# Performance work log

Measured on AMD Instinct MI355X. Metric: run time of the kernel, lower is better.

Reference implementation:

```python
import jax, jax.numpy as jnp
import numpy as np

N_NODES = 100_000
N_EDGES = 3_200_000
FAN_IN, FAN_MID, FAN_OUT = 512, 256, 64
NEG_SLOPE = 0.01  # F.leaky_relu default


def setup_inputs() -> dict:
    key = jax.random.key(0)
    ks = jax.random.split(key, 8)
    x = jax.random.normal(ks[0], (N_NODES, FAN_IN), dtype=jnp.float32)
    edge_src = jax.random.randint(ks[1], (N_EDGES,), 0, N_NODES, dtype=jnp.int32)
    edge_dst = jax.random.randint(ks[2], (N_EDGES,), 0, N_NODES, dtype=jnp.int32)
    edge_w1 = jax.random.uniform(ks[3], (N_EDGES,), dtype=jnp.float32)
    edge_w2 = jax.random.uniform(ks[4], (N_EDGES,), dtype=jnp.float32)
    W1 = jax.random.normal(ks[5], (FAN_IN, FAN_MID), dtype=jnp.float32) * (1.0 / np.sqrt(FAN_IN))
    b1 = jnp.zeros((FAN_MID,), dtype=jnp.float32)
    W2 = jax.random.normal(ks[6], (FAN_MID, FAN_OUT), dtype=jnp.float32) * (1.0 / np.sqrt(FAN_MID))
    b2 = jnp.zeros((FAN_OUT,), dtype=jnp.float32)
    return {"x": x, "edge_src": edge_src, "edge_dst": edge_dst,
            "edge_w1": edge_w1, "edge_w2": edge_w2,
            "W1": W1, "b1": b1, "W2": W2, "b2": b2}


def _gcn_layer(x, W, b, src, dst, ew):
    # GraphConvolution: support = x @ W ; out = A @ support + b (A sparse via edges)
    support = x @ W                                 # [N, F_out]
    msgs = support[src] * ew[:, None]               # gather + scale, [E, F_out]
    agg = jax.ops.segment_sum(msgs, dst, num_segments=x.shape[0])  # scatter-add
    return agg + b


def reference(x, edge_src, edge_dst, edge_w1, edge_w2, W1, b1, W2, b2):
    h = _gcn_layer(x, W1, b1, edge_src, edge_dst, edge_w1)
    h = jax.nn.leaky_relu(h, NEG_SLOPE)
    # dropout is identity at inference (training=False)
    h = _gcn_layer(h, W2, b2, edge_src, edge_dst, edge_w2)
    return jax.nn.log_softmax(h, axis=1)
```

## Files before the change

kernel.cpp:

```cpp
#include <hip/hip_runtime.h>
#include <stdint.h>

#define FAN_IN  512
#define FAN_MID 256
#define FAN_OUT 64
#define NEG_SLOPE 0.01f
#define NPB 128
#define MAXNB 1024
#define BPART 256

typedef __bf16 bf16_t;
typedef bf16_t bf16x8 __attribute__((ext_vector_type(8)));
typedef float  f32x4  __attribute__((ext_vector_type(4)));
typedef unsigned short u16x8 __attribute__((ext_vector_type(8)));

__device__ inline unsigned short f2b(float f) {
    union { float f; unsigned int u; } v; v.f = f;
    unsigned int u = v.u;
    return (unsigned short)((u + 0x7fffu + ((u >> 16) & 1u)) >> 16);
}
__device__ inline float b2f(unsigned short u) {
    union { unsigned int u; float f; } v; v.u = ((unsigned int)u) << 16; return v.f;
}

__global__ void zerob_kernel(int* p, int n) {
    int i = blockIdx.x * 256 + threadIdx.x;
    if (i < n) p[i] = 0;
}

__global__ __launch_bounds__(256) void part_hist(const int* __restrict__ dst,
                                                 int* __restrict__ gcount,
                                                 int* __restrict__ bcount,
                                                 int E, int nb, int chunk) {
    __shared__ int lc[MAXNB];
    int blk = blockIdx.x;
    for (int i = threadIdx.x; i < nb; i += 256) lc[i] = 0;
    __syncthreads();
    int s = blk * chunk;
    int e = s + chunk; if (e > E) e = E;
    for (int i = s + threadIdx.x; i < e; i += 256)
        atomicAdd(&lc[dst[i] >> 7], 1);
    __syncthreads();
    for (int i = threadIdx.x; i < nb; i += 256) {
        int c = lc[i];
        gcount[blk * nb + i] = c;
        if (c) atomicAdd(&bcount[i], c);
    }
}

__global__ void bscan_kernel(const int* __restrict__ bcount, int* __restrict__ boff,
                             int nb, int E) {
    __shared__ int part[1024];
    int t = threadIdx.x;
    int chunk = (nb + 1023) >> 10;
    int s = t * chunk;
    int e = s + chunk; if (e > nb) e = nb;
    int sum = 0;
    for (int i = s; i < e; i++) sum += bcount[i];
    part[t] = sum;
    __syncthreads();
    for (int off = 1; off < 1024; off <<= 1) {
        int v = (t >= off) ? part[t - off] : 0;
        __syncthreads();
        part[t] += v;
        __syncthreads();
    }
    int run = (t == 0) ? 0 : part[t - 1];
    for (int i = s; i < e; i++) {
        boff[i] = run;
        run += bcount[i];
    }
    if (t == 1023) boff[nb] = E;
}

__global__ __launch_bounds__(BPART) void part_scan(const int* __restrict__ gcount,
                                                   const int* __restrict__ boff,
                                                   int* __restrict__ gbase, int nb) {
    __shared__ int v[BPART];
    int bucket = blockIdx.x;
    int t = threadIdx.x;
    int val = gcount[t * nb + bucket];
    v[t] = val;
    __syncthreads();
    for (int off = 1; off < BPART; off <<= 1) {
        int x = (t >= off) ? v[t - off] : 0;
        __syncthreads();
        v[t] += x;
        __syncthreads();
    }
    gbase[t * nb + bucket] = (t == 0 ? 0 : v[t - 1]) + boff[bucket];
}

__global__ __launch_bounds__(256) void part_scatter(const int* __restrict__ src,
                                                    const int* __restrict__ dst,
                                                    const float* __restrict__ w1,
                                                    const float* __restrict__ w2,
                                                    const int* __restrict__ gbase,
                                                    uint4* __restrict__ bstage,
                                                    int E, int nb, int chunk) {
    __shared__ int lcur[MAXNB];
    int blk = blockIdx.x;
    for (int i = threadIdx.x; i < nb; i += 256) lcur[i] = gbase[blk * nb + i];
    __syncthreads();
    int s = blk * chunk;
    int e = s + chunk; if (e > E) e = E;
    for (int i = s + threadIdx.x; i < e; i += 256) {
        int d = dst[i];
        int pos = atomicAdd(&lcur[d >> 7], 1);
        uint4 v;
        v.x = (unsigned int)src[i];
        v.y = __float_as_uint(w1[i]);
        v.z = __float_as_uint(w2[i]);
        v.w = (unsigned int)d;
        bstage[pos] = v;
    }
}

__global__ __launch_bounds__(256) void bsort_kernel(const uint4* __restrict__ bstage,
                                                    const int* __restrict__ boff,
                                                    int* __restrict__ offsets,
                                                    uint4* __restrict__ csr,
                                                    int Nn, int E, int nb) {
    __shared__ int cnt[NPB];
    __shared__ int scn[NPB];
    __shared__ int cur[NPB];
    int b = blockIdx.x;
    int t = threadIdx.x;
    int base = boff[b], end = boff[b + 1];
    int n0 = b * NPB;
    if (t < NPB) cnt[t] = 0;
    __syncthreads();
    for (int i = base + t; i < end; i += 256)
        atomicAdd(&cnt[bstage[i].w - n0], 1);
    __syncthreads();
    if (t == 0) {
        int run = 0;
        for (int j = 0; j < NPB; j++) { scn[j] = run; run += cnt[j]; }
    }
    __syncthreads();
    if (t < NPB) {
        cur[t] = scn[t];
        int n = n0 + t;
        if (n < Nn) offsets[n] = base + scn[t];
    }
    if (b == nb - 1 && t == 0) offsets[Nn] = E;
    __syncthreads();
    for (int i = base + t; i < end; i += 256) {
        uint4 rec = bstage[i];
        int lp = atomicAdd(&cur[rec.w - n0], 1);
        csr[base + lp] = rec;
    }
}

__global__ void convert_w_kernel(const float* __restrict__ W, unsigned short* __restrict__ Wt,
                                 int K, int N) {
    int idx = blockIdx.x * 256 + threadIdx.x;
    if (idx >= K * N) return;
    int k = idx / N, n = idx % N;
    Wt[(size_t)n * K + k] = f2b(W[idx]);
}

template<int K, int N, bool A_F32>
__global__ __launch_bounds__(256) void gemm_bt(const void* __restrict__ Ap,
                                               const unsigned short* __restrict__ Bt,
                                               unsigned short* __restrict__ C, int M) {
    constexpr int LDT = 40;
    constexpr int NW  = N / 64;
    __shared__ unsigned short As[64 * LDT];
    __shared__ unsigned short Bs[N * LDT];
    const int m0   = blockIdx.x * 64;
    const int tid  = threadIdx.x;
    const int lane = tid & 63;
    const int w    = tid >> 6;
    const int lrow = tid >> 2;
    const int lseg = (tid & 3) * 8;
    const int q    = lane >> 4;
    const int mm   = lane & 15;

    f32x4 acc[4][NW] = {};

    for (int k0 = 0; k0 < K; k0 += 32) {
        __syncthreads();
        {
            int gm = m0 + lrow;
            u16x8 av;
            if (A_F32) {
                const float* A32 = (const float*)Ap;
                if (gm < M) {
                    const float4* pp = (const float4*)(A32 + (size_t)gm * K + k0 + lseg);
                    float4 f0 = pp[0], f1 = pp[1];
                    av[0] = f2b(f0.x); av[1] = f2b(f0.y); av[2] = f2b(f0.z); av[3] = f2b(f0.w);
                    av[4] = f2b(f1.x); av[5] = f2b(f1.y); av[6] = f2b(f1.z); av[7] = f2b(f1.w);
                } else av = (u16x8)0;
            } else {
                const unsigned short* A16 = (const unsigned short*)Ap;
                if (gm < M) av = *(const u16x8*)(A16 + (size_t)gm * K + k0 + lseg);
                else        av = (u16x8)0;
            }
            *(u16x8*)&As[lrow * LDT + lseg] = av;
        }
#pragma unroll
        for (int r = 0; r < N / 64; r++) {
            int nr = r * 64 + lrow;
            *(u16x8*)&Bs[nr * LDT + lseg] =
                *(const u16x8*)(Bt + (size_t)nr * K + k0 + lseg);
        }
        __syncthreads();

        bf16x8 a[4], b[NW];
#pragma unroll
        for (int mi = 0; mi < 4; mi++)
            a[mi] = *(const bf16x8*)&As[(mi * 16 + mm) * LDT + q * 8];
#pragma unroll
        for (int ni = 0; ni < NW; ni++)
            b[ni] = *(const bf16x8*)&Bs[(w * NW * 16 + ni * 16 + mm) * LDT + q * 8];
#pragma unroll
        for (int mi = 0; mi < 4; mi++)
#pragma unroll
            for (int ni = 0; ni < NW; ni++)
                acc[mi][ni] = __builtin_amdgcn_mfma_f32_16x16x32_bf16(a[mi], b[ni], acc[mi][ni], 0, 0, 0);
    }

#pragma unroll
    for (int mi = 0; mi < 4; mi++)
#pragma unroll
        for (int ni = 0; ni < NW; ni++)
#pragma unroll
            for (int r = 0; r < 4; r++) {
                int row = m0 + mi * 16 + q * 4 + r;
                if (row < M)
                    C[(size_t)row * N + w * NW * 16 + ni * 16 + mm] = f2b(acc[mi][ni][r]);
            }
}

__global__ __launch_bounds__(256) void agg1_kernel(const unsigned short* __restrict__ S,
                                                   const int* __restrict__ offsets,
                                                   const uint4* __restrict__ edges,
                                                   const float* __restrict__ b1,
                                                   unsigned short* __restrict__ h, int Nn) {
    int wave = threadIdx.x >> 6;
    int lane = threadIdx.x & 63;
    int node = blockIdx.x * 4 + wave;
    if (node >= Nn) return;
    int s = offsets[node], e = offsets[node + 1];
    float a0 = 0.f, a1 = 0.f, a2 = 0.f, a3 = 0.f;
    int i = s;
    for (; i + 4 <= e; i += 4) {
        uint4 e0 = edges[i], e1 = edges[i + 1], e2 = edges[i + 2], e3 = edges[i + 3];
        ushort4 v0 = *(const ushort4*)(S + (size_t)e0.x * 256 + lane * 4);
        ushort4 v1 = *(const ushort4*)(S + (size_t)e1.x * 256 + lane * 4);
        ushort4 v2 = *(const ushort4*)(S + (size_t)e2.x * 256 + lane * 4);
        ushort4 v3 = *(const ushort4*)(S + (size_t)e3.x * 256 + lane * 4);
        float w0 = __uint_as_float(e0.y), w1 = __uint_as_float(e1.y);
        float w2 = __uint_as_float(e2.y), w3 = __uint_as_float(e3.y);
        a0 += w0 * b2f(v0.x) + w1 * b2f(v1.x) + w2 * b2f(v2.x) + w3 * b2f(v3.x);
        a1 += w0 * b2f(v0.y) + w1 * b2f(v1.y) + w2 * b2f(v2.y) + w3 * b2f(v3.y);
        a2 += w0 * b2f(v0.z) + w1 * b2f(v1.z) + w2 * b2f(v2.z) + w3 * b2f(v3.z);
        a3 += w0 * b2f(v0.w) + w1 * b2f(v1.w) + w2 * b2f(v2.w) + w3 * b2f(v3.w);
    }
    for (; i < e; i++) {
        uint4 ev = edges[i];
        float w = __uint_as_float(ev.y);
        ushort4 v = *(const ushort4*)(S + (size_t)ev.x * 256 + lane * 4);
        a0 += w * b2f(v.x); a1 += w * b2f(v.y); a2 += w * b2f(v.z); a3 += w * b2f(v.w);
    }
    float4 bb = ((const float4*)b1)[lane];
    float r0 = a0 + bb.x, r1 = a1 + bb.y, r2 = a2 + bb.z, r3 = a3 + bb.w;
    r0 = r0 > 0.f ? r0 : r0 * NEG_SLOPE;
    r1 = r1 > 0.f ? r1 : r1 * NEG_SLOPE;
    r2 = r2 > 0.f ? r2 : r2 * NEG_SLOPE;
    r3 = r3 > 0.f ? r3 : r3 * NEG_SLOPE;
    ushort4 o;
    o.x = f2b(r0); o.y = f2b(r1); o.z = f2b(r2); o.w = f2b(r3);
    *(ushort4*)&h[(size_t)node * 256 + lane * 4] = o;
}

__global__ __launch_bounds__(256) void agg2_kernel(const unsigned short* __restrict__ S,
                                                   const int* __restrict__ offsets,
                                                   const uint4* __restrict__ edges,
                                                   const float* __restrict__ b2,
                                                   float* __restrict__ out, int Nn) {
    int wave = threadIdx.x >> 6;
    int lane = threadIdx.x & 63;
    int node = blockIdx.x * 4 + wave;
    if (node >= Nn) return;
    int s = offsets[node], e = offsets[node + 1];
    float acc = 0.f;
    int i = s;
    for (; i + 4 <= e; i += 4) {
        uint4 e0 = edges[i], e1 = edges[i + 1], e2 = edges[i + 2], e3 = edges[i + 3];
        float v0 = b2f(S[(size_t)e0.x * 64 + lane]);
        float v1 = b2f(S[(size_t)e1.x * 64 + lane]);
        float v2 = b2f(S[(size_t)e2.x * 64 + lane]);
        float v3 = b2f(S[(size_t)e3.x * 64 + lane]);
        acc += __uint_as_float(e0.z) * v0 + __uint_as_float(e1.z) * v1
             + __uint_as_float(e2.z) * v2 + __uint_as_float(e3.z) * v3;
    }
    for (; i < e; i++) {
        uint4 ev = edges[i];
        acc += __uint_as_float(ev.z) * b2f(S[(size_t)ev.x * 64 + lane]);
    }
    float logit = acc + b2[lane];
    float m = logit;
    for (int off = 32; off; off >>= 1) m = fmaxf(m, __shfl_xor(m, off));
    float ex = expf(logit - m);
    float sum = ex;
    for (int off = 32; off; off >>= 1) sum += __shfl_xor(sum, off);
    out[(size_t)node * 64 + lane] = logit - m - logf(sum);
}

extern "C" void kernel_launch(void* const* d_in, const int* in_sizes, int n_in,
                              void* d_out, int out_size, void* d_ws, size_t ws_size,
                              hipStream_t stream) {
    const float* x    = (const float*)d_in[0];
    const int*   esrc = (const int*)d_in[1];
    const int*   edst = (const int*)d_in[2];
    const float* ew1  = (const float*)d_in[3];
    const float* ew2  = (const float*)d_in[4];
    const float* W1   = (const float*)d_in[5];
    const float* b1   = (const float*)d_in[6];
    const float* W2   = (const float*)d_in[7];
    const float* b2   = (const float*)d_in[8];
    float* out = (float*)d_out;
    const int Nn = in_sizes[0] / FAN_IN;
    const int E  = in_sizes[1];
    const int NB = (Nn + NPB - 1) / NPB;
    const int chunk = (E + BPART - 1) / BPART;

    char* p = (char*)d_ws;
    auto alloc = [&](size_t bytes) -> char* {
        char* r = p;
        p += (bytes + 255) & ~(size_t)255;
        return r;
    };
    size_t s1_bytes = (size_t)Nn * FAN_MID * 2;
    size_t st_bytes = (size_t)E * 16;
    char* s1_region = alloc(s1_bytes > st_bytes ? s1_bytes : st_bytes);
    unsigned short* support1 = (unsigned short*)s1_region;
    uint4*          bstage   = (uint4*)s1_region;
    unsigned short* h        = (unsigned short*)alloc((size_t)Nn * FAN_MID * 2);
    unsigned short* support2 = (unsigned short*)alloc((size_t)Nn * FAN_OUT * 2);
    unsigned short* W1t      = (unsigned short*)alloc((size_t)FAN_IN * FAN_MID * 2);
    unsigned short* W2t      = (unsigned short*)alloc((size_t)FAN_MID * FAN_OUT * 2);
    int*            bcount   = (int*)alloc((size_t)NB * 4);
    int*            boff     = (int*)alloc(((size_t)NB + 1) * 4);
    int*            gcount   = (int*)alloc((size_t)BPART * NB * 4);
    int*            gbase    = (int*)alloc((size_t)BPART * NB * 4);
    int*            offsets  = (int*)alloc(((size_t)Nn + 1) * 4);
    uint4*          csr      = (uint4*)alloc((size_t)E * 16);

    zerob_kernel<<<(NB + 255) / 256, 256, 0, stream>>>(bcount, NB);
    part_hist<<<BPART, 256, 0, stream>>>(edst, gcount, bcount, E, NB, chunk);
    bscan_kernel<<<1, 1024, 0, stream>>>(bcount, boff, NB, E);
    part_scan<<<NB, BPART, 0, stream>>>(gcount, boff, gbase, NB);
    part_scatter<<<BPART, 256, 0, stream>>>(esrc, edst, ew1, ew2, gbase, bstage, E, NB, chunk);
    bsort_kernel<<<NB, 256, 0, stream>>>(bstage, boff, offsets, csr, Nn, E, NB);

    convert_w_kernel<<<(FAN_IN * FAN_MID + 255) / 256, 256, 0, stream>>>(W1, W1t, FAN_IN, FAN_MID);
    convert_w_kernel<<<(FAN_MID * FAN_OUT + 255) / 256, 256, 0, stream>>>(W2, W2t, FAN_MID, FAN_OUT);

    gemm_bt<FAN_IN, FAN_MID, true><<<dim3((Nn + 63) / 64, 1), 256, 0, stream>>>(
        x, W1t, support1, Nn);
    agg1_kernel<<<(Nn + 3) / 4, 256, 0, stream>>>(support1, offsets, csr, b1, h, Nn);

    gemm_bt<FAN_MID, FAN_OUT, false><<<dim3((Nn + 63) / 64, 1), 256, 0, stream>>>(
        h, W2t, support2, Nn);
    agg2_kernel<<<(Nn + 3) / 4, 256, 0, stream>>>(support2, offsets, csr, b2, out, Nn);
}
```

Before: 868.7 us.

## Split CSR edge records into per-layer 8-byte arrays and unroll gathers by eight

The sort kernel now writes two 8-byte edge arrays, (src, w1) and (src, w2), in place of one 16-byte record. Each aggregation kernel reads only the array it needs, which halves the edge-record traffic that every lane of the wave loads. Both aggregation loops add an 8-wide unrolled path that issues all edge and feature loads before accumulating, to keep more gathers in flight. The cost is one extra store stream in bsort, plus higher register pressure and a different floating-point summation order.

Result: no change. 859.6 us (-1.0%).

```diff
diff --git a/kernel.cpp b/kernel.cpp
--- a/kernel.cpp
+++ b/kernel.cpp
@@ -119,7 +119,8 @@
 __global__ __launch_bounds__(256) void bsort_kernel(const uint4* __restrict__ bstage,
                                                     const int* __restrict__ boff,
                                                     int* __restrict__ offsets,
-                                                    uint4* __restrict__ csr,
+                                                    uint2* __restrict__ csr1,
+                                                    uint2* __restrict__ csr2,
                                                     int Nn, int E, int nb) {
     __shared__ int cnt[NPB];
     __shared__ int scn[NPB];
@@ -148,7 +149,10 @@
     for (int i = base + t; i < end; i += 256) {
         uint4 rec = bstage[i];
         int lp = atomicAdd(&cur[rec.w - n0], 1);
-        csr[base + lp] = rec;
+        uint2 r1; r1.x = rec.x; r1.y = rec.y;
+        uint2 r2; r2.x = rec.x; r2.y = rec.z;
+        csr1[base + lp] = r1;
+        csr2[base + lp] = r2;
     }
 }
 
@@ -235,7 +239,7 @@
 
 __global__ __launch_bounds__(256) void agg1_kernel(const unsigned short* __restrict__ S,
                                                    const int* __restrict__ offsets,
-                                                   const uint4* __restrict__ edges,
+                                                   const uint2* __restrict__ edges,
                                                    const float* __restrict__ b1,
                                                    unsigned short* __restrict__ h, int Nn) {
     int wave = threadIdx.x >> 6;
@@ -245,21 +249,42 @@
     int s = offsets[node], e = offsets[node + 1];
     float a0 = 0.f, a1 = 0.f, a2 = 0.f, a3 = 0.f;
     int i = s;
+    for (; i + 8 <= e; i += 8) {
+        uint2 ed[8];
+#pragma unroll
+        for (int j = 0; j < 8; j++) ed[j] = edges[i + j];
+        ushort4 v[8];
+#pragma unroll
+        for (int j = 0; j < 8; j++)
+            v[j] = *(const ushort4*)(S + (size_t)ed[j].x * 256 + lane * 4);
+#pragma unroll
+        for (int j = 0; j < 8; j++) {
+            float w = __uint_as_float(ed[j].y);
+            a0 += w * b2f(v[j].x);
+            a1 += w * b2f(v[j].y);
+            a2 += w * b2f(v[j].z);
+            a3 += w * b2f(v[j].w);
+        }
+    }
     for (; i + 4 <= e; i += 4) {
-        uint4 e0 = edges[i], e1 = edges[i + 1], e2 = edges[i + 2], e3 = edges[i + 3];
-        ushort4 v0 = *(const ushort4*)(S + (size_t)e0.x * 256 + lane * 4);
-        ushort4 v1 = *(const ushort4*)(S + (size_t)e1.x * 256 + lane * 4);
-        ushort4 v2 = *(const ushort4*)(S + (size_t)e2.x * 256 + lane * 4);
-        ushort4 v3 = *(const ushort4*)(S + (size_t)e3.x * 256 + lane * 4);
-        float w0 = __uint_as_float(e0.y), w1 = __uint_as_float(e1.y);
-        float w2 = __uint_as_float(e2.y), w3 = __uint_as_float(e3.y);
-        a0 += w0 * b2f(v0.x) + w1 * b2f(v1.x) + w2 * b2f(v2.x) + w3 * b2f(v3.x);
-        a1 += w0 * b2f(v0.y) + w1 * b2f(v1.y) + w2 * b2f(v2.y) + w3 * b2f(v3.y);
-        a2 += w0 * b2f(v0.z) + w1 * b2f(v1.z) + w2 * b2f(v2.z) + w3 * b2f(v3.z);
-        a3 += w0 * b2f(v0.w) + w1 * b2f(v1.w) + w2 * b2f(v2.w) + w3 * b2f(v3.w);
+        uint2 ed[4];
+#pragma unroll
+        for (int j = 0; j < 4; j++) ed[j] = edges[i + j];
+        ushort4 v[4];
+#pragma unroll
+        for (int j = 0; j < 4; j++)
+            v[j] = *(const ushort4*)(S + (size_t)ed[j].x * 256 + lane * 4);
+#pragma unroll
+        for (int j = 0; j < 4; j++) {
+            float w = __uint_as_float(ed[j].y);
+            a0 += w * b2f(v[j].x);
+            a1 += w * b2f(v[j].y);
+            a2 += w * b2f(v[j].z);
+            a3 += w * b2f(v[j].w);
+        }
     }
     for (; i < e; i++) {
-        uint4 ev = edges[i];
+        uint2 ev = edges[i];
         float w = __uint_as_float(ev.y);
         ushort4 v = *(const ushort4*)(S + (size_t)ev.x * 256 + lane * 4);
         a0 += w * b2f(v.x); a1 += w * b2f(v.y); a2 += w * b2f(v.z); a3 += w * b2f(v.w);
@@ -277,7 +302,7 @@
 
 __global__ __launch_bounds__(256) void agg2_kernel(const unsigned short* __restrict__ S,
                                                    const int* __restrict__ offsets,
-                                                   const uint4* __restrict__ edges,
+                                                   const uint2* __restrict__ edges,
                                                    const float* __restrict__ b2,
                                                    float* __restrict__ out, int Nn) {
     int wave = threadIdx.x >> 6;
@@ -287,18 +312,33 @@
     int s = offsets[node], e = offsets[node + 1];
     float acc = 0.f;
     int i = s;
+    for (; i + 8 <= e; i += 8) {
+        uint2 ed[8];
+#pragma unroll
+        for (int j = 0; j < 8; j++) ed[j] = edges[i + j];
+        float v[8];
+#pragma unroll
+        for (int j = 0; j < 8; j++)
+            v[j] = b2f(S[(size_t)ed[j].x * 64 + lane]);
+#pragma unroll
+        for (int j = 0; j < 8; j++)
+            acc += __uint_as_float(ed[j].y) * v[j];
+    }
     for (; i + 4 <= e; i += 4) {
-        uint4 e0 = edges[i], e1 = edges[i + 1], e2 = edges[i + 2], e3 = edges[i + 3];
-        float v0 = b2f(S[(size_t)e0.x * 64 + lane]);
-        float v1 = b2f(S[(size_t)e1.x * 64 + lane]);
-        float v2 = b2f(S[(size_t)e2.x * 64 + lane]);
-        float v3 = b2f(S[(size_t)e3.x * 64 + lane]);
-        acc += __uint_as_float(e0.z) * v0 + __uint_as_float(e1.z) * v1
-             + __uint_as_float(e2.z) * v2 + __uint_as_float(e3.z) * v3;
+        uint2 ed[4];
+#pragma unroll
+        for (int j = 0; j < 4; j++) ed[j] = edges[i + j];
+        float v[4];
+#pragma unroll
+        for (int j = 0; j < 4; j++)
+            v[j] = b2f(S[(size_t)ed[j].x * 64 + lane]);
+#pragma unroll
+        for (int j = 0; j < 4; j++)
+            acc += __uint_as_float(ed[j].y) * v[j];
     }
     for (; i < e; i++) {
-        uint4 ev = edges[i];
-        acc += __uint_as_float(ev.z) * b2f(S[(size_t)ev.x * 64 + lane]);
+        uint2 ev = edges[i];
+        acc += __uint_as_float(ev.y) * b2f(S[(size_t)ev.x * 64 + lane]);
     }
     float logit = acc + b2[lane];
     float m = logit;
@@ -347,23 +387,24 @@
     int*            gcount   = (int*)alloc((size_t)BPART * NB * 4);
     int*            gbase    = (int*)alloc((size_t)BPART * NB * 4);
     int*            offsets  = (int*)alloc(((size_t)Nn + 1) * 4);
-    uint4*          csr      = (uint4*)alloc((size_t)E * 16);
+    uint2*          csr1     = (uint2*)alloc((size_t)E * 8);
+    uint2*          csr2     = (uint2*)alloc((size_t)E * 8);
 
     zerob_kernel<<<(NB + 255) / 256, 256, 0, stream>>>(bcount, NB);
     part_hist<<<BPART, 256, 0, stream>>>(edst, gcount, bcount, E, NB, chunk);
     bscan_kernel<<<1, 1024, 0, stream>>>(bcount, boff, NB, E);
     part_scan<<<NB, BPART, 0, stream>>>(gcount, boff, gbase, NB);
     part_scatter<<<BPART, 256, 0, stream>>>(esrc, edst, ew1, ew2, gbase, bstage, E, NB, chunk);
-    bsort_kernel<<<NB, 256, 0, stream>>>(bstage, boff, offsets, csr, Nn, E, NB);
+    bsort_kernel<<<NB, 256, 0, stream>>>(bstage, boff, offsets, csr1, csr2, Nn, E, NB);
 
     convert_w_kernel<<<(FAN_IN * FAN_MID + 255) / 256, 256, 0, stream>>>(W1, W1t, FAN_IN, FAN_MID);
     convert_w_kernel<<<(FAN_MID * FAN_OUT + 255) / 256, 256, 0, stream>>>(W2, W2t, FAN_MID, FAN_OUT);
 
     gemm_bt<FAN_IN, FAN_MID, true><<<dim3((Nn + 63) / 64, 1), 256, 0, stream>>>(
         x, W1t, support1, Nn);
-    agg1_kernel<<<(Nn + 3) / 4, 256, 0, stream>>>(support1, offsets, csr, b1, h, Nn);
+    agg1_kernel<<<(Nn + 3) / 4, 256, 0, stream>>>(support1, offsets, csr1, b1, h, Nn);
 
     gemm_bt<FAN_MID, FAN_OUT, false><<<dim3((Nn + 63) / 64, 1), 256, 0, stream>>>(
         h, W2t, support2, Nn);
-    agg2_kernel<<<(Nn + 3) / 4, 256, 0, stream>>>(support2, offsets, csr, b2, out, Nn);
-}
+    agg2_kernel<<<(Nn + 3) / 4, 256, 0, stream>>>(support2, offsets, csr2, b2, out, Nn);
+}
```
